# Performance work log

Measured on AMD Instinct MI355X. Metric: run time of the kernel, lower is better.

Reference implementation:

```python
import jax, jax.numpy as jnp
import numpy as np

N_QUBITS = 12
DEPTH = 3


def _apply_1q(state, U, wire, n):
    # state: [B, 2^n] complex; U: [2,2] (shared) or [B,2,2] (per-sample)
    B = state.shape[0]
    a = 2 ** wire
    c = 2 ** (n - wire - 1)
    psi = state.reshape(B, a, 2, c)
    if U.ndim == 2:
        psi = jnp.einsum('ij,bajc->baic', U, psi)
    else:
        psi = jnp.einsum('bij,bajc->baic', U, psi)
    return psi.reshape(B, -1)


def _apply_cnot(state, ctrl, tgt, n):
    B = state.shape[0]
    psi = state.reshape((B,) + (2,) * n)
    psi = jnp.moveaxis(psi, (1 + ctrl, 1 + tgt), (1, 2))
    # flip target bit on the control=1 branch
    psi = jnp.concatenate([psi[:, :1], jnp.flip(psi[:, 1:], axis=2)], axis=1)
    psi = jnp.moveaxis(psi, (1, 2), (1 + ctrl, 1 + tgt))
    return psi.reshape(B, -1)


def _ry(theta):
    # theta: [B] -> [B,2,2]
    c = jnp.cos(theta / 2)
    s = jnp.sin(theta / 2)
    return jnp.stack([jnp.stack([c, -s], -1), jnp.stack([s, c], -1)], -2).astype(jnp.complex64)


def _rot(phi, theta, omega):
    # PennyLane Rot(phi, theta, omega) = RZ(omega) @ RY(theta) @ RZ(phi)
    c = jnp.cos(theta / 2).astype(jnp.complex64)
    s = jnp.sin(theta / 2).astype(jnp.complex64)
    e = lambda a: jnp.exp(1j * a.astype(jnp.complex64))
    m00 = e(-(phi + omega) / 2) * c
    m01 = -e((phi - omega) / 2) * s
    m10 = e(-(phi - omega) / 2) * s
    m11 = e((phi + omega) / 2) * c
    return jnp.stack([jnp.stack([m00, m01]), jnp.stack([m10, m11])])


def _circuit(angles, weights, n, depth):
    # angles: [B, n] real; weights: [depth, n, 3]
    B = angles.shape[0]
    state = jnp.zeros((B, 2 ** n), jnp.complex64).at[:, 0].set(1.0)
    # RY angle encoding
    for q in range(n):
        state = _apply_1q(state, _ry(angles[:, q]), q, n)
    # StronglyEntanglingLayers: Rot on each wire, then ring CNOTs with range r
    for l in range(depth):
        for q in range(n):
            U = _rot(weights[l, q, 0], weights[l, q, 1], weights[l, q, 2])
            state = _apply_1q(state, U, q, n)
        r = l % (n - 1) + 1  # PennyLane default ranges
        for q in range(n):
            state = _apply_cnot(state, q, (q + r) % n, n)
    # PauliZ expectation on each wire
    probs = state.real ** 2 + state.imag ** 2  # [B, 2^n]
    idx = jnp.arange(2 ** n)
    bits = (idx[None, :] >> (n - 1 - jnp.arange(n)[:, None])) & 1  # wire 0 = MSB
    signs = (1.0 - 2.0 * bits).astype(probs.dtype)  # [n, 2^n]
    return probs @ signs.T  # [B, n]


def setup_inputs() -> dict:
    key = jax.random.key(0)
    ks = jax.random.split(key, 5)
    B, F, n, C = 4096, 768, N_QUBITS, 10
    x = jax.random.normal(ks[0], (B, F), jnp.float32)
    Wp = jax.random.normal(ks[1], (n, F), jnp.float32) / np.sqrt(F)
    weights = 0.01 * jax.random.normal(ks[2], (DEPTH, n, 3), jnp.float32)
    Wo = jax.random.normal(ks[3], (C, n), jnp.float32) / np.sqrt(n)
    bo = jax.random.normal(ks[4], (C,), jnp.float32) * 0.01
    return {'x': x, 'Wp': Wp, 'weights': weights, 'Wo': Wo, 'bo': bo}


def reference(x, Wp, weights, Wo, bo):
    angles = jnp.tanh(x @ Wp.T) * (np.pi / 2)  # [B, n_qubits]
    z = _circuit(angles, weights, N_QUBITS, DEPTH)  # [B, n_qubits]
    return z @ Wo.T + bo  # [B, num_classes]
```

## Files before the change

kernel.cpp:

```cpp
#include <hip/hip_runtime.h>
#include <math.h>

#define NQ 12
#define DEPTH 3
#define FEAT 768
#define NCLS 10
#define NW 8
#define AMPS 8
#define PI_HALF 1.57079632679489662f

typedef float v2f __attribute__((ext_vector_type(2)));

__device__ __forceinline__ v2f pk_mul_bl(v2f A, v2f z) {
    v2f d;
    asm("v_pk_mul_f32 %0, %1, %2 op_sel:[0,0] op_sel_hi:[1,0]"
        : "=v"(d) : "v"(A), "v"(z));
    return d;
}
__device__ __forceinline__ void pk_fma_bl(v2f& d, v2f A, v2f z) {
    asm("v_pk_fma_f32 %0, %1, %2, %0 op_sel:[0,0,0] op_sel_hi:[1,0,1]"
        : "+v"(d) : "v"(A), "v"(z));
}
__device__ __forceinline__ void pk_fma_bh(v2f& d, v2f B, v2f z) {
    asm("v_pk_fma_f32 %0, %1, %2, %0 op_sel:[0,1,0] op_sel_hi:[1,1,1]"
        : "+v"(d) : "v"(B), "v"(z));
}
__device__ __forceinline__ v2f cgate(v2f As, v2f Bs, v2f Ap, v2f Bp, v2f z, v2f p) {
    v2f d = pk_mul_bl(As, z);
    pk_fma_bh(d, Bs, z);
    pk_fma_bl(d, Ap, p);
    pk_fma_bh(d, Bp, p);
    return d;
}

#define DPPF(v, ctrl) __int_as_float(__builtin_amdgcn_update_dpp(0, __float_as_int(v), (ctrl), 0xF, 0xF, true))

template<int M>
__device__ __forceinline__ float swx(float v) {
    if constexpr (M == 1) {
        return DPPF(v, 0xB1);
    } else if constexpr (M == 2) {
        return DPPF(v, 0x4E);
    } else if constexpr (M == 4) {
        float t = DPPF(v, 0x141);
        return DPPF(t, 0x1B);
    } else if constexpr (M == 8) {
        return DPPF(v, 0x128);
    } else if constexpr (M == 16) {
        return __int_as_float(__builtin_amdgcn_ds_swizzle(__float_as_int(v), 0x401F));
    } else {
        return __shfl_xor(v, 32, 64);
    }
}

template<int M>
__device__ __forceinline__ v2f swx2(v2f z) {
    v2f p;
    p.x = swx<M>(z.x);
    p.y = swx<M>(z.y);
    return p;
}

__device__ __forceinline__ float allred(float v) {
    v += swx<1>(v); v += swx<2>(v); v += swx<4>(v);
    v += swx<8>(v); v += swx<16>(v); v += swx<32>(v);
    return v;
}


template<int JM>
__device__ __forceinline__ void rot_reg(v2f (&z)[AMPS], const v2f* m) {
    const v2f A0 = m[0], B0 = m[1], P0 = m[2], Q0 = m[3];
    const v2f A1 = m[4], B1 = m[5], P1 = m[6], Q1 = m[7];
    #pragma unroll
    for (int j = 0; j < AMPS; ++j) if (!(j & JM)) {
        const int j1 = j | JM;
        v2f z0 = z[j], z1 = z[j1];
        z[j]  = cgate(A0, B0, P0, Q0, z0, z1);
        z[j1] = cgate(A1, B1, P1, Q1, z1, z0);
    }
}

template<int LM>
__device__ __forceinline__ void rot_lane(v2f (&z)[AMPS], const v2f* m, int lane) {
    const bool b = (lane & LM) != 0;
    const v2f As = b ? m[4] : m[0], Bs = b ? m[5] : m[1];
    const v2f Ap = b ? m[6] : m[2], Bp = b ? m[7] : m[3];
    #pragma unroll
    for (int j = 0; j < AMPS; ++j) {
        v2f p = swx2<LM>(z[j]);
        z[j] = cgate(As, Bs, Ap, Bp, z[j], p);
    }
}

__device__ __forceinline__ void relayout(v2f (&z)[AMPS], v2f (*ex)[AMPS][64], int lw, int lane) {
    #pragma unroll
    for (int k = 0; k < AMPS; ++k) ex[lw][k][lane] = z[k];
    __syncthreads();
    #pragma unroll
    for (int k = 0; k < AMPS; ++k) z[k] = ex[k][lw][lane];
    __syncthreads();
}

__device__ __forceinline__ void exch_89(v2f (&z)[AMPS], v2f (*ex)[AMPS][64], int lw, int lane) {
    #pragma unroll
    for (int k = 0; k < AMPS; ++k) ex[lw][k][lane] = z[k];
    __syncthreads();
    if (lane & 1) {
        #pragma unroll
        for (int k = 0; k < AMPS; ++k) z[k] = ex[lw ^ 4][k][lane];
    }
    __syncthreads();
}

__device__ __forceinline__ void exch_10_11(v2f (&z)[AMPS], v2f (*ex)[AMPS][64], int lw, int lane) {
    #pragma unroll
    for (int k = 0; k < AMPS; ++k) ex[lw][k][lane] = z[k];
    __syncthreads();
    #pragma unroll
    for (int k = 0; k < AMPS; ++k) {
        const int so = (k & 3) << 1;
        if (so) z[k] = ex[lw ^ so][k][lane];
    }
    __syncthreads();
}

template<int JC, int JT>
__device__ __forceinline__ void cnot_rr(v2f (&z)[AMPS]) {
    #pragma unroll
    for (int j = 0; j < AMPS; ++j) if ((j & JC) && !(j & JT)) {
        const int j1 = j | JT;
        v2f t = z[j]; z[j] = z[j1]; z[j1] = t;
    }
}

template<int JC, int LT>
__device__ __forceinline__ void cnot_rl(v2f (&z)[AMPS]) {
    #pragma unroll
    for (int j = 0; j < AMPS; ++j) if (j & JC) z[j] = swx2<LT>(z[j]);
}

template<int LC, int JT>
__device__ __forceinline__ void cnot_lr(v2f (&z)[AMPS], int lane) {
    const bool b = (lane & LC) != 0;
    #pragma unroll
    for (int j = 0; j < AMPS; ++j) if (!(j & JT)) {
        const int j1 = j | JT;
        v2f z0 = z[j], z1 = z[j1];
        z[j]  = b ? z1 : z0;
        z[j1] = b ? z0 : z1;
    }
}

template<int LC, int LT>
__device__ __forceinline__ void cnot_ll(v2f (&z)[AMPS], int lane) {
    const bool b = (lane & LC) != 0;
    #pragma unroll
    for (int j = 0; j < AMPS; ++j) {
        v2f p = swx2<LT>(z[j]);
        z[j] = b ? p : z[j];
    }
}

template<int PC, int LT>
__device__ __forceinline__ void cnot_wl(v2f (&z)[AMPS], int lw) {
    if (lw & PC) {
        #pragma unroll
        for (int j = 0; j < AMPS; ++j) z[j] = swx2<LT>(z[j]);
    }
}

template<int PC, int JT>
__device__ __forceinline__ void cnot_wr(v2f (&z)[AMPS], int lw) {
    if (lw & PC) {
        #pragma unroll
        for (int j = 0; j < AMPS; ++j) if (!(j & JT)) {
            const int j1 = j | JT;
            v2f t = z[j]; z[j] = z[j1]; z[j1] = t;
        }
    }
}

__global__ __launch_bounds__(512) void qcircuit_rl(
    const float* __restrict__ x,
    const float* __restrict__ Wp,
    const float* __restrict__ w,
    const float* __restrict__ Wo,
    const float* __restrict__ bo,
    float* __restrict__ out)
{
    const int t = threadIdx.x;
    const int wave = t >> 6;
    const int lane = t & 63;
    const int b = blockIdx.x;

    __shared__ v2f mcoef[DEPTH * NQ][8];
    __shared__ v2f ex[NW][AMPS][64];
    __shared__ float red[NW][NQ];
    __shared__ float sh_dot[NQ];
    __shared__ float sh_ac[NQ], sh_as[NQ], zsh[NQ];

    if (t < DEPTH * NQ) {
        float phi = w[t * 3 + 0], th = w[t * 3 + 1], om = w[t * 3 + 2];
        float ct = cosf(0.5f * th), sn = sinf(0.5f * th);
        float a0 = -0.5f * (phi + om);
        float a1 = 0.5f * (phi - om);
        float c0 = cosf(a0), s0 = sinf(a0);
        float c1 = cosf(a1), s1 = sinf(a1);
        float m00r = c0 * ct,  m00i = s0 * ct;
        float m01r = -c1 * sn, m01i = -s1 * sn;
        float m10r = c1 * sn,  m10i = -s1 * sn;
        float m11r = c0 * ct,  m11i = -s0 * ct;
        mcoef[t][0] = v2f{m00r, m00i};  mcoef[t][1] = v2f{-m00i, m00r};
        mcoef[t][2] = v2f{m01r, m01i};  mcoef[t][3] = v2f{-m01i, m01r};
        mcoef[t][4] = v2f{m11r, m11i};  mcoef[t][5] = v2f{-m11i, m11r};
        mcoef[t][6] = v2f{m10r, m10i};  mcoef[t][7] = v2f{-m10i, m10r};
    }

    {
        const float2* x2  = reinterpret_cast<const float2*>(x + (size_t)b * FEAT);
        const float2* Wp2 = reinterpret_cast<const float2*>(Wp);
        float2 xv[6];
        #pragma unroll
        for (int c = 0; c < 6; ++c) xv[c] = x2[lane + 64 * c];
        float accA = 0.f;
        #pragma unroll
        for (int c = 0; c < 6; ++c) {
            float2 wv = Wp2[wave * 384 + lane + 64 * c];
            accA += xv[c].x * wv.x + xv[c].y * wv.y;
        }
        accA = allred(accA);
        float accB = 0.f;
        if (wave < 4) {
            #pragma unroll
            for (int c = 0; c < 6; ++c) {
                float2 wv = Wp2[(wave + 8) * 384 + lane + 64 * c];
                accB += xv[c].x * wv.x + xv[c].y * wv.y;
            }
            accB = allred(accB);
        }
        if (lane == 0) {
            sh_dot[wave] = accA;
            if (wave < 4) sh_dot[wave + 8] = accB;
        }
    }
    __syncthreads();
    if (t < NQ) {
        float h = 0.5f * (tanhf(sh_dot[t]) * PI_HALF);
        sh_ac[t] = cosf(h);
        sh_as[t] = sinf(h);
    }
    __syncthreads();

    int lw = wave;
    float pr[AMPS];
    float L = ((wave & 4) ? sh_as[0] : sh_ac[0]);
    L *= (wave & 2) ? sh_as[1] : sh_ac[1];
    L *= (wave & 1) ? sh_as[2] : sh_ac[2];
    L *= (lane & 32) ? sh_as[3] : sh_ac[3];
    L *= (lane & 16) ? sh_as[4] : sh_ac[4];
    L *= (lane &  8) ? sh_as[5] : sh_ac[5];
    L *= (lane &  4) ? sh_as[6] : sh_ac[6];
    L *= (lane &  2) ? sh_as[7] : sh_ac[7];
    L *= (lane &  1) ? sh_as[8] : sh_ac[8];
    pr[0] = L;
    #pragma unroll
    for (int wbit = 0; wbit < 3; ++wbit) {
        const int bmask = 1 << wbit;
        const float cw = sh_ac[11 - wbit], sw = sh_as[11 - wbit];
        #pragma unroll
        for (int j = 0; j < AMPS; ++j) {
            if (j < bmask) {
                pr[j | bmask] = pr[j] * sw;
                pr[j] = pr[j] * cw;
            }
        }
    }
    v2f z[AMPS];
    #pragma unroll
    for (int j = 0; j < AMPS; ++j) z[j] = v2f{pr[j], 0.f};

    {
        const v2f* mb = &mcoef[0 * NQ][0];
        rot_reg < 4>(z, mb + 9 * 8);
        rot_reg < 2>(z, mb + 10 * 8);
        rot_reg < 1>(z, mb + 11 * 8);
        rot_lane<32>(z, mb + 3 * 8, lane);
        rot_lane<16>(z, mb + 4 * 8, lane);
        rot_lane< 8>(z, mb + 5 * 8, lane);
        rot_lane< 4>(z, mb + 6 * 8, lane);
        rot_lane< 2>(z, mb + 7 * 8, lane);
        rot_lane< 1>(z, mb + 8 * 8, lane);
        relayout(z, ex, lw, lane);
        rot_reg < 4>(z, mb + 0 * 8);
        rot_reg < 2>(z, mb + 1 * 8);
        rot_reg < 1>(z, mb + 2 * 8);
        cnot_rr< 4,  2>(z);
        cnot_rr< 2,  1>(z);
        cnot_rl< 1, 32>(z);
        cnot_ll<32, 16>(z, lane);
        cnot_ll<16,  8>(z, lane);
        cnot_ll< 8,  4>(z, lane);
        cnot_ll< 4,  2>(z, lane);
        cnot_ll< 2,  1>(z, lane);
        exch_89(z, ex, lw, lane);
        lw ^= (lw & 4) ? 2 : 0;
        lw ^= (lw & 2) ? 1 : 0;
        cnot_wr< 1,  4>(z, lw);
    }
    {
        const v2f* mb = &mcoef[1 * NQ][0];
        rot_reg < 4>(z, mb + 0 * 8);
        rot_reg < 2>(z, mb + 1 * 8);
        rot_reg < 1>(z, mb + 2 * 8);
        rot_lane<32>(z, mb + 3 * 8, lane);
        rot_lane<16>(z, mb + 4 * 8, lane);
        rot_lane< 8>(z, mb + 5 * 8, lane);
        rot_lane< 4>(z, mb + 6 * 8, lane);
        rot_lane< 2>(z, mb + 7 * 8, lane);
        rot_lane< 1>(z, mb + 8 * 8, lane);
        relayout(z, ex, lw, lane);
        rot_reg < 4>(z, mb + 9 * 8);
        rot_reg < 2>(z, mb + 10 * 8);
        rot_reg < 1>(z, mb + 11 * 8);
        lw ^= (lw & 4) ? 1 : 0;
        cnot_wl< 2, 32>(z, lw);
        cnot_wl< 1, 16>(z, lw);
        cnot_ll<32,  8>(z, lane);
        cnot_ll<16,  4>(z, lane);
        cnot_ll< 8,  2>(z, lane);
        cnot_ll< 4,  1>(z, lane);
        cnot_lr< 2,  4>(z, lane);
        cnot_lr< 1,  2>(z, lane);
        cnot_rr< 4,  1>(z);
        exch_10_11(z, ex, lw, lane);
    }
    {
        const v2f* mb = &mcoef[2 * NQ][0];
        rot_reg < 4>(z, mb + 9 * 8);
        rot_reg < 2>(z, mb + 10 * 8);
        rot_reg < 1>(z, mb + 11 * 8);
        rot_lane<32>(z, mb + 3 * 8, lane);
        rot_lane<16>(z, mb + 4 * 8, lane);
        rot_lane< 8>(z, mb + 5 * 8, lane);
        rot_lane< 4>(z, mb + 6 * 8, lane);
        rot_lane< 2>(z, mb + 7 * 8, lane);
        rot_lane< 1>(z, mb + 8 * 8, lane);
        relayout(z, ex, lw, lane);
        rot_reg < 4>(z, mb + 0 * 8);
        rot_reg < 2>(z, mb + 1 * 8);
        rot_reg < 1>(z, mb + 2 * 8);
    }

    float ptot = 0.f, zn4 = 0.f, zn2 = 0.f, zn1 = 0.f;
    #pragma unroll
    for (int j = 0; j < AMPS; ++j) {
        float p = z[j].x * z[j].x + z[j].y * z[j].y;
        ptot += p;
        if (j & 4) zn4 += p;
        if (j & 2) zn2 += p;
        if (j & 1) zn1 += p;
    }
    const float S4 = ptot - 2.f * zn4;
    const float S2 = ptot - 2.f * zn2;
    const float S1 = ptot - 2.f * zn1;
    const bool p36 = ((lane >> 5) ^ (lane >> 2)) & 1;
    const bool p18 = ((lane >> 4) ^ (lane >> 1)) & 1;
    const bool p9  = ((lane >> 3) ^ lane) & 1;

    const float a0 = allred(p36 ? -ptot : ptot);
    const float a1 = allred(p18 ? -ptot : ptot);
    const float a2 = allred(p9  ? -ptot : ptot);
    const float a3 = allred((lane & 32) ? -S4 : S4);
    const float a4 = allred((lane & 16) ? -S2 : S2);
    const float a5 = allred((lane &  8) ? -S1 : S1);
    const float a6 = allred(p36 ? -S4 : S4);
    const float a7 = allred(p18 ? -S2 : S2);
    const float a8 = allred(p9  ? -S1 : S1);

    const float W9  = (lw & 4) ? -1.f : 1.f;
    const float W10 = (lw & 2) ? -1.f : 1.f;
    const float W11 = (lw & 1) ? -1.f : 1.f;
    float zp[NQ];
    zp[0]  = W9 * a0;   zp[1]  = W10 * a1;  zp[2]  = W11 * a2;
    zp[3]  = a3;        zp[4]  = a4;        zp[5]  = a5;
    zp[6]  = a6;        zp[7]  = a7;        zp[8]  = a8;
    zp[9]  = W9 * a6;   zp[10] = W10 * a7;  zp[11] = W11 * a8;

    if (lane == 0) {
        #pragma unroll
        for (int q = 0; q < NQ; ++q) red[wave][q] = zp[q];
    }
    __syncthreads();
    if (t < NQ) {
        float s = 0.f;
        #pragma unroll
        for (int v = 0; v < NW; ++v) s += red[v][t];
        zsh[t] = s;
    }
    __syncthreads();

    if (t < NCLS) {
        float o = bo[t];
        #pragma unroll
        for (int q = 0; q < NQ; ++q) o = fmaf(zsh[q], Wo[t * NQ + q], o);
        out[(size_t)b * NCLS + t] = o;
    }
}

extern "C" void kernel_launch(void* const* d_in, const int* in_sizes, int n_in,
                              void* d_out, int out_size, void* d_ws, size_t ws_size,
                              hipStream_t stream) {
    const float* x  = (const float*)d_in[0];
    const float* Wp = (const float*)d_in[1];
    const float* w  = (const float*)d_in[2];
    const float* Wo = (const float*)d_in[3];
    const float* bo = (const float*)d_in[4];
    float* out = (float*)d_out;

    const int B = in_sizes[0] / FEAT;
    qcircuit_rl<<<B, 512, 0, stream>>>(x, Wp, w, Wo, bo, out);
}
```

Measured before the change: 155.3 us.

## Fold CNOT ring permutations into LDS exchange gather indices

Replaces the per-layer chains of CNOT gates (register swaps, cross-lane shuffles and wave-conditional swaps) plus the separate exchange steps with a single LDS store/gather per layer. The gather addresses compose the whole CNOT permutation over wave, register and lane bits. This removes many DPP/permute instructions and selects. The cost is more complex, possibly bank-conflicting LDS read addresses, and the index algebra must reproduce the permutation exactly.

```diff
diff --git a/kernel.cpp b/kernel.cpp
--- a/kernel.cpp
+++ b/kernel.cpp
@@ -102,29 +102,6 @@
     __syncthreads();
 }
 
-__device__ __forceinline__ void exch_89(v2f (&z)[AMPS], v2f (*ex)[AMPS][64], int lw, int lane) {
-    #pragma unroll
-    for (int k = 0; k < AMPS; ++k) ex[lw][k][lane] = z[k];
-    __syncthreads();
-    if (lane & 1) {
-        #pragma unroll
-        for (int k = 0; k < AMPS; ++k) z[k] = ex[lw ^ 4][k][lane];
-    }
-    __syncthreads();
-}
-
-__device__ __forceinline__ void exch_10_11(v2f (&z)[AMPS], v2f (*ex)[AMPS][64], int lw, int lane) {
-    #pragma unroll
-    for (int k = 0; k < AMPS; ++k) ex[lw][k][lane] = z[k];
-    __syncthreads();
-    #pragma unroll
-    for (int k = 0; k < AMPS; ++k) {
-        const int so = (k & 3) << 1;
-        if (so) z[k] = ex[lw ^ so][k][lane];
-    }
-    __syncthreads();
-}
-
 template<int JC, int JT>
 __device__ __forceinline__ void cnot_rr(v2f (&z)[AMPS]) {
     #pragma unroll
@@ -134,54 +111,7 @@
     }
 }
 
-template<int JC, int LT>
-__device__ __forceinline__ void cnot_rl(v2f (&z)[AMPS]) {
-    #pragma unroll
-    for (int j = 0; j < AMPS; ++j) if (j & JC) z[j] = swx2<LT>(z[j]);
-}
-
-template<int LC, int JT>
-__device__ __forceinline__ void cnot_lr(v2f (&z)[AMPS], int lane) {
-    const bool b = (lane & LC) != 0;
-    #pragma unroll
-    for (int j = 0; j < AMPS; ++j) if (!(j & JT)) {
-        const int j1 = j | JT;
-        v2f z0 = z[j], z1 = z[j1];
-        z[j]  = b ? z1 : z0;
-        z[j1] = b ? z0 : z1;
-    }
-}
-
-template<int LC, int LT>
-__device__ __forceinline__ void cnot_ll(v2f (&z)[AMPS], int lane) {
-    const bool b = (lane & LC) != 0;
-    #pragma unroll
-    for (int j = 0; j < AMPS; ++j) {
-        v2f p = swx2<LT>(z[j]);
-        z[j] = b ? p : z[j];
-    }
-}
-
-template<int PC, int LT>
-__device__ __forceinline__ void cnot_wl(v2f (&z)[AMPS], int lw) {
-    if (lw & PC) {
-        #pragma unroll
-        for (int j = 0; j < AMPS; ++j) z[j] = swx2<LT>(z[j]);
-    }
-}
-
-template<int PC, int JT>
-__device__ __forceinline__ void cnot_wr(v2f (&z)[AMPS], int lw) {
-    if (lw & PC) {
-        #pragma unroll
-        for (int j = 0; j < AMPS; ++j) if (!(j & JT)) {
-            const int j1 = j | JT;
-            v2f t = z[j]; z[j] = z[j1]; z[j1] = t;
-        }
-    }
-}
-
-__global__ __launch_bounds__(512) void qcircuit_rl(
+__global__ __launch_bounds__(512) void qcircuit_fz(
     const float* __restrict__ x,
     const float* __restrict__ Wp,
     const float* __restrict__ w,
@@ -254,16 +184,16 @@
 
     int lw = wave;
     float pr[AMPS];
-    float L = ((wave & 4) ? sh_as[0] : sh_ac[0]);
-    L *= (wave & 2) ? sh_as[1] : sh_ac[1];
-    L *= (wave & 1) ? sh_as[2] : sh_ac[2];
-    L *= (lane & 32) ? sh_as[3] : sh_ac[3];
-    L *= (lane & 16) ? sh_as[4] : sh_ac[4];
-    L *= (lane &  8) ? sh_as[5] : sh_ac[5];
-    L *= (lane &  4) ? sh_as[6] : sh_ac[6];
-    L *= (lane &  2) ? sh_as[7] : sh_ac[7];
-    L *= (lane &  1) ? sh_as[8] : sh_ac[8];
-    pr[0] = L;
+    float L0 = ((wave & 4) ? sh_as[0] : sh_ac[0]);
+    L0 *= (wave & 2) ? sh_as[1] : sh_ac[1];
+    L0 *= (wave & 1) ? sh_as[2] : sh_ac[2];
+    L0 *= (lane & 32) ? sh_as[3] : sh_ac[3];
+    L0 *= (lane & 16) ? sh_as[4] : sh_ac[4];
+    L0 *= (lane &  8) ? sh_as[5] : sh_ac[5];
+    L0 *= (lane &  4) ? sh_as[6] : sh_ac[6];
+    L0 *= (lane &  2) ? sh_as[7] : sh_ac[7];
+    L0 *= (lane &  1) ? sh_as[8] : sh_ac[8];
+    pr[0] = L0;
     #pragma unroll
     for (int wbit = 0; wbit < 3; ++wbit) {
         const int bmask = 1 << wbit;
@@ -297,16 +227,26 @@
         rot_reg < 1>(z, mb + 2 * 8);
         cnot_rr< 4,  2>(z);
         cnot_rr< 2,  1>(z);
-        cnot_rl< 1, 32>(z);
-        cnot_ll<32, 16>(z, lane);
-        cnot_ll<16,  8>(z, lane);
-        cnot_ll< 8,  4>(z, lane);
-        cnot_ll< 4,  2>(z, lane);
-        cnot_ll< 2,  1>(z, lane);
-        exch_89(z, ex, lw, lane);
-        lw ^= (lw & 4) ? 2 : 0;
-        lw ^= (lw & 2) ? 1 : 0;
-        cnot_wr< 1,  4>(z, lw);
+        {
+            const int woff = (lane & 1) << 2;
+            int Ls = lane;
+            Ls ^= (Ls & 2) >> 1;
+            Ls ^= (Ls & 4) >> 1;
+            Ls ^= (Ls & 8) >> 1;
+            Ls ^= (Ls & 16) >> 1;
+            Ls ^= (Ls & 32) >> 1;
+            int lw2 = lw ^ ((lw & 4) ? 2 : 0);
+            lw2 ^= (lw2 & 2) ? 1 : 0;
+            const int wlc = (lw2 & 1) << 2;
+            #pragma unroll
+            for (int k = 0; k < AMPS; ++k) ex[lw][k][lane] = z[k];
+            __syncthreads();
+            #pragma unroll
+            for (int k = 0; k < AMPS; ++k)
+                z[k] = ex[lw ^ woff][k ^ wlc][Ls ^ ((k & 1) << 5)];
+            __syncthreads();
+            lw = lw2;
+        }
     }
     {
         const v2f* mb = &mcoef[1 * NQ][0];
@@ -323,17 +263,26 @@
         rot_reg < 4>(z, mb + 9 * 8);
         rot_reg < 2>(z, mb + 10 * 8);
         rot_reg < 1>(z, mb + 11 * 8);
-        lw ^= (lw & 4) ? 1 : 0;
-        cnot_wl< 2, 32>(z, lw);
-        cnot_wl< 1, 16>(z, lw);
-        cnot_ll<32,  8>(z, lane);
-        cnot_ll<16,  4>(z, lane);
-        cnot_ll< 8,  2>(z, lane);
-        cnot_ll< 4,  1>(z, lane);
-        cnot_lr< 2,  4>(z, lane);
-        cnot_lr< 1,  2>(z, lane);
-        cnot_rr< 4,  1>(z);
-        exch_10_11(z, ex, lw, lane);
+        {
+            lw ^= (lw & 4) >> 2;
+            int Ls = lane;
+            Ls ^= (Ls & 4) >> 2;
+            Ls ^= (Ls & 8) >> 2;
+            Ls ^= (Ls & 16) >> 2;
+            Ls ^= (Ls & 32) >> 2;
+            const int klx = ((lane & 2) << 1) ^ ((lane & 1) << 1);
+            #pragma unroll
+            for (int k = 0; k < AMPS; ++k) ex[lw][k][lane] = z[k];
+            __syncthreads();
+            #pragma unroll
+            for (int k = 0; k < AMPS; ++k) {
+                const int LW = lw ^ ((k & 1) << 1) ^ ((k & 2) << 1);
+                const int K  = k ^ ((k & 4) >> 2) ^ klx;
+                const int Lr = Ls ^ ((LW & 1) << 4) ^ ((LW & 2) << 4);
+                z[k] = ex[LW][K][Lr];
+            }
+            __syncthreads();
+        }
     }
     {
         const v2f* mb = &mcoef[2 * NQ][0];
@@ -419,5 +368,5 @@
     float* out = (float*)d_out;
 
     const int B = in_sizes[0] / FEAT;
-    qcircuit_rl<<<B, 512, 0, stream>>>(x, Wp, w, Wo, bo, out);
-}
+    qcircuit_fz<<<B, 512, 0, stream>>>(x, Wp, w, Wo, bo, out);
+}
```

Result: faster. 128.9 us (-17.0%).
